# Kernel tuning notes

Hardware: AMD Instinct MI355X
Metric: run time of the kernel (lower is better)

## Reference

```python
import jax, jax.numpy as jnp
import numpy as np

N_NODES = 100000
N_EDGES = 3200000
IN_C, HID, OUT_C = 128, 256, 128
N_GRAPHS = 64
EPS = 1e-5


def setup_inputs() -> dict:
    key = jax.random.key(0)
    ks = jax.random.split(key, 16)
    x = jax.random.normal(ks[0], (N_NODES, IN_C), dtype=jnp.float32)
    edge_index = jax.random.randint(ks[1], (2, N_EDGES), 0, N_NODES, dtype=jnp.int64 if jax.config.jax_enable_x64 else jnp.int32)
    batch = jnp.sort(jax.random.randint(ks[2], (N_NODES,), 0, N_GRAPHS, dtype=jnp.int32))
    def glorot(k, shape):
        lim = jnp.sqrt(6.0 / (shape[-2] + shape[-1]))
        return jax.random.uniform(k, shape, jnp.float32, -lim, lim)
    return {
        "x": x,
        "W_in": glorot(ks[3], (IN_C, HID)),
        "b_in": jnp.zeros((HID,), jnp.float32),
        "g_in": jnp.ones((HID,), jnp.float32),
        "be_in": jnp.zeros((HID,), jnp.float32),
        "W_hid": glorot(ks[4], (2, HID, HID)),
        "b_hid": jnp.zeros((2, HID), jnp.float32),
        "g_hid": jnp.ones((2, HID), jnp.float32),
        "be_hid": jnp.zeros((2, HID), jnp.float32),
        "W_out": glorot(ks[5], (HID, OUT_C)),
        "b_out": jnp.zeros((OUT_C,), jnp.float32),
        "g_out": jnp.ones((OUT_C,), jnp.float32),
        "be_out": jnp.zeros((OUT_C,), jnp.float32),
        "edge_index": edge_index,
        "batch": batch,
    }


def _gcn_norm(edge_index, n_nodes):
    # add self-loops, symmetric deg^-1/2 normalization (PyG GCNConv defaults)
    loop = jnp.arange(n_nodes, dtype=edge_index.dtype)
    src = jnp.concatenate([edge_index[0], loop])
    dst = jnp.concatenate([edge_index[1], loop])
    deg = jax.ops.segment_sum(jnp.ones_like(dst, dtype=jnp.float32), dst, num_segments=n_nodes)
    dinv = jnp.where(deg > 0, jax.lax.rsqrt(deg), 0.0)
    norm = dinv[src] * dinv[dst]  # [E+N]
    return src, dst, norm


def _block(x, W, b, g, be, src, dst, norm, n_nodes):
    h = x @ W  # [N, out]
    agg = jax.ops.segment_sum(h[src] * norm[:, None], dst, num_segments=n_nodes) + b
    a = jax.nn.leaky_relu(agg, negative_slope=0.01)
    mu = jnp.mean(a, axis=0)
    var = jnp.mean(jnp.square(a - mu), axis=0)
    return (a - mu) * jax.lax.rsqrt(var + EPS) * g + be


def reference(x, W_in, b_in, g_in, be_in, W_hid, b_hid, g_hid, be_hid,
              W_out, b_out, g_out, be_out, edge_index, batch):
    n = x.shape[0]
    src, dst, norm = _gcn_norm(edge_index, n)
    h = _block(x, W_in, b_in, g_in, be_in, src, dst, norm, n)
    for i in range(W_hid.shape[0]):
        h = _block(h, W_hid[i], b_hid[i], g_hid[i], be_hid[i], src, dst, norm, n)
    h = _block(h, W_out, b_out, g_out, be_out, src, dst, norm, n)
    # global mean pool over graphs
    sums = jax.ops.segment_sum(h, batch, num_segments=N_GRAPHS)
    cnts = jax.ops.segment_sum(jnp.ones((n,), h.dtype), batch, num_segments=N_GRAPHS)
    return sums / jnp.maximum(cnts, 1.0)[:, None]
```

## Files before the change

### kernel.cpp

```cpp
#include <hip/hip_runtime.h>
#include <stdint.h>

#define EPS_LN 1e-5f

typedef short bf16x8 __attribute__((ext_vector_type(8)));
typedef float f32x4  __attribute__((ext_vector_type(4)));

__device__ __forceinline__ unsigned short f2bf(float f) {
    unsigned u = __float_as_uint(f);
    unsigned r = (u + 0x7fffu + ((u >> 16) & 1u)) >> 16;
    return (unsigned short)r;
}
__device__ __forceinline__ float bf_lo(unsigned u) { return __uint_as_float(u << 16); }
__device__ __forceinline__ float bf_hi(unsigned u) { return __uint_as_float(u & 0xffff0000u); }

__device__ __forceinline__ void async16(void* lds, const void* g) {
    __builtin_amdgcn_global_load_lds(
        (const __attribute__((address_space(1))) unsigned int*)g,
        (__attribute__((address_space(3))) unsigned int*)lds, 16, 0, 0);
}


__global__ void count_deg_kernel(const int* __restrict__ dst, int E, unsigned* __restrict__ deg) {
    int e = blockIdx.x * blockDim.x + threadIdx.x;
    if (e < E) atomicAdd(&deg[dst[e]], 1u);
}

__global__ void block_sums_kernel(const unsigned* __restrict__ deg, unsigned* __restrict__ part, int N) {
    __shared__ unsigned s[256];
    int t = threadIdx.x;
    int i0 = blockIdx.x * 512 + t * 2;
    unsigned a = (i0 < N) ? deg[i0] : 0u;
    unsigned b = (i0 + 1 < N) ? deg[i0 + 1] : 0u;
    s[t] = a + b;
    __syncthreads();
    for (int off = 128; off > 0; off >>= 1) {
        if (t < off) s[t] += s[t + off];
        __syncthreads();
    }
    if (t == 0) part[blockIdx.x] = s[0];
}

__global__ void scan_part_kernel(unsigned* __restrict__ part, unsigned* __restrict__ row_ptr,
                                 int NB, int N) {
    __shared__ unsigned s[256];
    int t = threadIdx.x;
    unsigned v = (t < NB) ? part[t] : 0u;
    s[t] = v;
    __syncthreads();
    for (int off = 1; off < 256; off <<= 1) {
        unsigned u = (t >= off) ? s[t - off] : 0u;
        __syncthreads();
        s[t] += u;
        __syncthreads();
    }
    if (t < NB) part[t] = s[t] - v;
    if (t == 255) row_ptr[N] = s[255];
}

__global__ void scan_blocks_kernel(const unsigned* __restrict__ deg, const unsigned* __restrict__ part,
                                   unsigned* __restrict__ row_ptr, unsigned* __restrict__ cursor,
                                   float* __restrict__ dinv, int N) {
    __shared__ unsigned s[256];
    int t = threadIdx.x;
    int i0 = blockIdx.x * 512 + t * 2;
    unsigned a = (i0 < N) ? deg[i0] : 0u;
    unsigned b = (i0 + 1 < N) ? deg[i0 + 1] : 0u;
    unsigned pair = a + b;
    s[t] = pair;
    __syncthreads();
    for (int off = 1; off < 256; off <<= 1) {
        unsigned u = (t >= off) ? s[t - off] : 0u;
        __syncthreads();
        s[t] += u;
        __syncthreads();
    }
    unsigned excl = s[t] - pair + part[blockIdx.x];
    if (i0 < N) {
        row_ptr[i0] = excl; cursor[i0] = excl;
        dinv[i0] = rsqrtf((float)(a + 1u));
    }
    if (i0 + 1 < N) {
        row_ptr[i0 + 1] = excl + a; cursor[i0 + 1] = excl + a;
        dinv[i0 + 1] = rsqrtf((float)(b + 1u));
    }
}

__global__ void fill_csr_kernel(const int* __restrict__ src, const int* __restrict__ dst,
                                const float* __restrict__ dinv, int E,
                                unsigned* __restrict__ cursor, uint2* __restrict__ csr) {
    int e = blockIdx.x * blockDim.x + threadIdx.x;
    if (e < E) {
        int d = dst[e];
        int s = src[e];
        unsigned pos = atomicAdd(&cursor[d], 1u);
        float w = dinv[d] * dinv[s];
        csr[pos] = make_uint2((unsigned)s, __float_as_uint(w));
    }
}

__global__ void prep_all_kernel(const float* __restrict__ x, unsigned* __restrict__ xbf,
                                const float* __restrict__ W_in, unsigned short* __restrict__ Wt_in,
                                const float* __restrict__ W_hid, unsigned short* __restrict__ Wt_h0,
                                unsigned short* __restrict__ Wt_h1, int n2) {
    int i = blockIdx.x * blockDim.x + threadIdx.x;
    if (i < n2) {
        float2 v = *reinterpret_cast<const float2*>(&x[(size_t)i * 2]);
        xbf[i] = (unsigned)f2bf(v.x) | ((unsigned)f2bf(v.y) << 16);
        return;
    }
    int r = i - n2;
    if (r < 32768) {
        int k = r >> 8, c = r & 255;
        Wt_in[(size_t)c * 128 + k] = f2bf(W_in[r]);
    } else if (r < 32768 + 65536) {
        r -= 32768;
        int k = r >> 8, c = r & 255;
        Wt_h0[(size_t)c * 256 + k] = f2bf(W_hid[r]);
    } else if (r < 32768 + 131072) {
        r -= 32768 + 65536;
        int k = r >> 8, c = r & 255;
        Wt_h1[(size_t)c * 256 + k] = f2bf(W_hid[65536 + r]);
    }
}

template<int UPL, bool AFF, bool FINAL>
__global__ void aggregate_bf(const unsigned* __restrict__ X, void* __restrict__ outp,
                             const unsigned* __restrict__ row_ptr, const uint2* __restrict__ csr,
                             const float* __restrict__ dinv,
                             const float* __restrict__ ssum, const float* __restrict__ ssq,
                             const float* __restrict__ gg, const float* __restrict__ be, float invN,
                             const float* __restrict__ tW, const float* __restrict__ bias, int N) {
    constexpr int C = UPL * 64;
    constexpr unsigned RSU = C / 2;
    constexpr int PC = UPL * 2;

    __shared__ float sL[AFF ? C : 1], tL[AFF ? C : 1];
    if constexpr (AFF) {
        for (int i = threadIdx.x; i < C; i += 256) {
            float mu = ssum[i] * invN;
            float var = ssq[i] * invN - mu * mu;
            float s = gg[i] * rsqrtf(var + EPS_LN);
            sL[i] = s;
            tL[i] = be[i] - mu * s;
        }
        __syncthreads();
    }

    int node = blockIdx.x * 8 + (threadIdx.x >> 5);
    if (node >= N) return;
    int ll = threadIdx.x & 31;
    unsigned cu = (unsigned)ll * UPL;

    float di = dinv[node];
    float w0 = di * di;
    float acc[PC];
    float wsum = w0;
    {
        const unsigned* xr = X + (size_t)((unsigned)node * RSU + cu);
        if constexpr (UPL == 4) {
            uint4 v = *reinterpret_cast<const uint4*>(xr);
            unsigned uu[4] = {v.x, v.y, v.z, v.w};
            #pragma unroll
            for (int q = 0; q < 4; ++q) {
                acc[q * 2 + 0] = w0 * bf_lo(uu[q]);
                acc[q * 2 + 1] = w0 * bf_hi(uu[q]);
            }
        } else {
            uint2 v = *reinterpret_cast<const uint2*>(xr);
            acc[0] = w0 * bf_lo(v.x); acc[1] = w0 * bf_hi(v.x);
            acc[2] = w0 * bf_lo(v.y); acc[3] = w0 * bf_hi(v.y);
        }
    }
    unsigned e0 = row_ptr[node];
    unsigned e1 = row_ptr[node + 1];
    unsigned cnt = e1 - e0;
    unsigned full = cnt & ~7u;

    for (unsigned i = 0; i < full; i += 8) {
        uint2 p[8];
        #pragma unroll
        for (int u = 0; u < 8; ++u) p[u] = csr[e0 + i + u];
        if constexpr (UPL == 4) {
            uint4 v[8];
            #pragma unroll
            for (int u = 0; u < 8; ++u)
                v[u] = *reinterpret_cast<const uint4*>(X + (size_t)(p[u].x * RSU + cu));
            #pragma unroll
            for (int u = 0; u < 8; ++u) {
                float f = __uint_as_float(p[u].y);
                unsigned uu[4] = {v[u].x, v[u].y, v[u].z, v[u].w};
                #pragma unroll
                for (int q = 0; q < 4; ++q) {
                    acc[q * 2 + 0] += f * bf_lo(uu[q]);
                    acc[q * 2 + 1] += f * bf_hi(uu[q]);
                }
                wsum += f;
            }
        } else {
            uint2 v[8];
            #pragma unroll
            for (int u = 0; u < 8; ++u)
                v[u] = *reinterpret_cast<const uint2*>(X + (size_t)(p[u].x * RSU + cu));
            #pragma unroll
            for (int u = 0; u < 8; ++u) {
                float f = __uint_as_float(p[u].y);
                acc[0] += f * bf_lo(v[u].x); acc[1] += f * bf_hi(v[u].x);
                acc[2] += f * bf_lo(v[u].y); acc[3] += f * bf_hi(v[u].y);
                wsum += f;
            }
        }
    }
    for (unsigned i = full; i < cnt; ++i) {
        uint2 p = csr[e0 + i];
        float f = __uint_as_float(p.y);
        if constexpr (UPL == 4) {
            uint4 v = *reinterpret_cast<const uint4*>(X + (size_t)(p.x * RSU + cu));
            unsigned uu[4] = {v.x, v.y, v.z, v.w};
            #pragma unroll
            for (int q = 0; q < 4; ++q) {
                acc[q * 2 + 0] += f * bf_lo(uu[q]);
                acc[q * 2 + 1] += f * bf_hi(uu[q]);
            }
        } else {
            uint2 v = *reinterpret_cast<const uint2*>(X + (size_t)(p.x * RSU + cu));
            acc[0] += f * bf_lo(v.x); acc[1] += f * bf_hi(v.x);
            acc[2] += f * bf_lo(v.y); acc[3] += f * bf_hi(v.y);
        }
        wsum += f;
    }

    int col = ll * PC;
    float z[PC];
    #pragma unroll
    for (int j = 0; j < PC; ++j) {
        float f = acc[j];
        if constexpr (AFF) f = sL[col + j] * f + tL[col + j] * wsum;
        if constexpr (FINAL) {
            f = f + wsum * tW[col + j] + bias[col + j];
            f = f > 0.f ? f : 0.01f * f;
        }
        z[j] = f;
    }
    if constexpr (FINAL) {
        float* of = (float*)outp;
        *reinterpret_cast<float4*>(&of[(size_t)node * C + col]) = make_float4(z[0], z[1], z[2], z[3]);
    } else {
        unsigned* ou = (unsigned*)outp;
        if constexpr (UPL == 4) {
            uint4 pk;
            pk.x = (unsigned)f2bf(z[0]) | ((unsigned)f2bf(z[1]) << 16);
            pk.y = (unsigned)f2bf(z[2]) | ((unsigned)f2bf(z[3]) << 16);
            pk.z = (unsigned)f2bf(z[4]) | ((unsigned)f2bf(z[5]) << 16);
            pk.w = (unsigned)f2bf(z[6]) | ((unsigned)f2bf(z[7]) << 16);
            *reinterpret_cast<uint4*>(&ou[(size_t)((unsigned)node * RSU + cu)]) = pk;
        } else {
            uint2 pk;
            pk.x = (unsigned)f2bf(z[0]) | ((unsigned)f2bf(z[1]) << 16);
            pk.y = (unsigned)f2bf(z[2]) | ((unsigned)f2bf(z[3]) << 16);
            *reinterpret_cast<uint2*>(&ou[(size_t)((unsigned)node * RSU + cu)]) = pk;
        }
    }
}

template<int K, int NN, bool EPI>
__launch_bounds__(256)
__global__ void gemm_mfma(const unsigned short* __restrict__ Z, const unsigned short* __restrict__ Wt,
                          const float* __restrict__ bias, unsigned short* __restrict__ out,
                          float* __restrict__ stat_sum, float* __restrict__ stat_sq, int M) {
    __shared__ char smem[32768];
    __shared__ float csum[128], csq[128];

    const int tid = threadIdx.x;
    const int lane = tid & 63;
    const int w = tid >> 6;
    const int wr = (w >> 1) * 64;
    const int wc = (w & 1) * 64;
    const int rowBase = blockIdx.x * 128;
    const int colBase = blockIdx.y * 128;
    const int frow = lane & 15;
    const int kgrp = lane >> 4;

    f32x4 acc[4][4] = {};

    for (int kt = 0; kt < K / 64; ++kt) {
        #pragma unroll
        for (int i = 0; i < 4; ++i) {
            int g = (i * 4 + w) * 64 + lane;
            int r = g >> 3;
            int bl = (g & 7) * 16;
            int bg = bl ^ ((r & 7) << 4);
            const char* src = (const char*)Z + (((size_t)(rowBase + r) * K + kt * 64) << 1) + bg;
            async16(&smem[(i * 4 + w) * 1024], src);
        }
        #pragma unroll
        for (int i = 0; i < 4; ++i) {
            int g = (i * 4 + w) * 64 + lane;
            int r = g >> 3;
            int bl = (g & 7) * 16;
            int bg = bl ^ ((r & 7) << 4);
            const char* src = (const char*)Wt + (((size_t)(colBase + r) * K + kt * 64) << 1) + bg;
            async16(&smem[16384 + (i * 4 + w) * 1024], src);
        }
        __syncthreads();
        #pragma unroll
        for (int kk = 0; kk < 2; ++kk) {
            const int kbyte = kk * 64 + kgrp * 16;
            bf16x8 af[4], bfr[4];
            #pragma unroll
            for (int m = 0; m < 4; ++m) {
                int r = wr + m * 16 + frow;
                af[m] = *reinterpret_cast<const bf16x8*>(&smem[r * 128 + (kbyte ^ ((r & 7) << 4))]);
            }
            #pragma unroll
            for (int n = 0; n < 4; ++n) {
                int c = wc + n * 16 + frow;
                bfr[n] = *reinterpret_cast<const bf16x8*>(&smem[16384 + c * 128 + (kbyte ^ ((c & 7) << 4))]);
            }
            #pragma unroll
            for (int m = 0; m < 4; ++m)
                #pragma unroll
                for (int n = 0; n < 4; ++n)
                    acc[m][n] = __builtin_amdgcn_mfma_f32_16x16x32_bf16(bfr[n], af[m], acc[m][n], 0, 0, 0);
        }
        __syncthreads();
    }

    if constexpr (EPI) {
        if (tid < 128) { csum[tid] = 0.f; csq[tid] = 0.f; }
        __syncthreads();
    }

    #pragma unroll
    for (int n = 0; n < 4; ++n) {
        const int c_local = wc + n * 16 + kgrp * 4;
        const int col = colBase + c_local;
        float4 b4 = make_float4(0.f, 0.f, 0.f, 0.f);
        if constexpr (EPI) b4 = *reinterpret_cast<const float4*>(&bias[col]);
        float ps[4] = {0.f, 0.f, 0.f, 0.f}, pq[4] = {0.f, 0.f, 0.f, 0.f};
        #pragma unroll
        for (int m = 0; m < 4; ++m) {
            int row = rowBase + wr + m * 16 + frow;
            if (row < M) {
                float f0 = acc[m][n][0] + b4.x;
                float f1 = acc[m][n][1] + b4.y;
                float f2 = acc[m][n][2] + b4.z;
                float f3 = acc[m][n][3] + b4.w;
                if constexpr (EPI) {
                    f0 = f0 > 0.f ? f0 : 0.01f * f0;
                    f1 = f1 > 0.f ? f1 : 0.01f * f1;
                    f2 = f2 > 0.f ? f2 : 0.01f * f2;
                    f3 = f3 > 0.f ? f3 : 0.01f * f3;
                }
                uint2 pk;
                pk.x = (unsigned)f2bf(f0) | ((unsigned)f2bf(f1) << 16);
                pk.y = (unsigned)f2bf(f2) | ((unsigned)f2bf(f3) << 16);
                *reinterpret_cast<uint2*>(&out[(size_t)row * NN + col]) = pk;
                if constexpr (EPI) {
                    ps[0] += f0; ps[1] += f1; ps[2] += f2; ps[3] += f3;
                    pq[0] += f0 * f0; pq[1] += f1 * f1; pq[2] += f2 * f2; pq[3] += f3 * f3;
                }
            }
        }
        if constexpr (EPI) {
            #pragma unroll
            for (int s = 1; s < 16; s <<= 1) {
                #pragma unroll
                for (int j = 0; j < 4; ++j) {
                    ps[j] += __shfl_xor(ps[j], s);
                    pq[j] += __shfl_xor(pq[j], s);
                }
            }
            if (frow == 0) {
                #pragma unroll
                for (int j = 0; j < 4; ++j) {
                    atomicAdd(&csum[c_local + j], ps[j]);
                    atomicAdd(&csq[c_local + j], pq[j]);
                }
            }
        }
    }
    if constexpr (EPI) {
        __syncthreads();
        if (tid < 128) {
            atomicAdd(&stat_sum[colBase + tid], csum[tid]);
            atomicAdd(&stat_sq[colBase + tid], csq[tid]);
        }
    }
}

__global__ void prep_wout_tw(const float* __restrict__ W,
                             const float* __restrict__ ssum, const float* __restrict__ ssq,
                             const float* __restrict__ gg, const float* __restrict__ be, float invN,
                             unsigned short* __restrict__ Wt, float* __restrict__ tW) {
    if (blockIdx.x < 128) {
        int idx = blockIdx.x * 256 + threadIdx.x;
        int k = idx >> 7, c = idx & 127;
        float mu = ssum[k] * invN;
        float var = ssq[k] * invN - mu * mu;
        float s = gg[k] * rsqrtf(var + EPS_LN);
        Wt[(size_t)c * 256 + k] = f2bf(s * W[idx]);
    } else {
        int c = threadIdx.x;
        if (c < 128) {
            float acc = 0.f;
            for (int k = 0; k < 256; ++k) {
                float mu = ssum[k] * invN;
                float var = ssq[k] * invN - mu * mu;
                float s = gg[k] * rsqrtf(var + EPS_LN);
                float t = be[k] - mu * s;
                acc += t * W[k * 128 + c];
            }
            tW[c] = acc;
        }
    }
}

__global__ void stats_pool_kernel(const float* __restrict__ A, const int* __restrict__ batch,
                                  float* __restrict__ stat_sum, float* __restrict__ stat_sq,
                                  float* __restrict__ psums, float* __restrict__ pcnt, int N) {
    int c = threadIdx.x;
    int n0 = blockIdx.x * 256;
    if (n0 >= N) return;
    int n1 = min(n0 + 256, N);
    float cs = 0.f, cq = 0.f;
    float acc = 0.f, cacc = 0.f;
    int curg = -1;
    for (int n = n0; n < n1; ++n) {
        float v = A[(size_t)n * 128 + c];
        cs += v; cq += v * v;
        int g = batch[n];
        if (g != curg) {
            if (curg >= 0) {
                atomicAdd(&psums[curg * 128 + c], acc);
                if (c == 0) atomicAdd(&pcnt[curg], cacc);
            }
            acc = 0.f; cacc = 0.f; curg = g;
        }
        acc += v;
        cacc += 1.f;
    }
    if (curg >= 0) {
        atomicAdd(&psums[curg * 128 + c], acc);
        if (c == 0) atomicAdd(&pcnt[curg], cacc);
    }
    atomicAdd(&stat_sum[c], cs);
    atomicAdd(&stat_sq[c], cq);
}

__global__ void divide_kernel(const float* __restrict__ psums, const float* __restrict__ pcnt,
                              const float* __restrict__ ssum, const float* __restrict__ ssq,
                              const float* __restrict__ gg, const float* __restrict__ be, float invN,
                              float* __restrict__ out) {
    int i = blockIdx.x * blockDim.x + threadIdx.x;
    if (i < 64 * 128) {
        int g = i >> 7, c = i & 127;
        float mu = ssum[c] * invN;
        float var = ssq[c] * invN - mu * mu;
        float s = gg[c] * rsqrtf(var + EPS_LN);
        float t = be[c] - mu * s;
        float cnt = pcnt[g];
        out[i] = (cnt > 0.f) ? s * (psums[i] / cnt) + t : 0.f;
    }
}

extern "C" void kernel_launch(void* const* d_in, const int* in_sizes, int n_in,
                              void* d_out, int out_size, void* d_ws, size_t ws_size,
                              hipStream_t stream) {
    const float* x      = (const float*)d_in[0];
    const float* W_in   = (const float*)d_in[1];
    const float* b_in   = (const float*)d_in[2];
    const float* g_in   = (const float*)d_in[3];
    const float* be_in  = (const float*)d_in[4];
    const float* W_hid  = (const float*)d_in[5];
    const float* b_hid  = (const float*)d_in[6];
    const float* g_hid  = (const float*)d_in[7];
    const float* be_hid = (const float*)d_in[8];
    const float* W_out  = (const float*)d_in[9];
    const float* b_out  = (const float*)d_in[10];
    const float* g_out  = (const float*)d_in[11];
    const float* be_out = (const float*)d_in[12];
    const int*   eidx   = (const int*)d_in[13];
    const int*   batch  = (const int*)d_in[14];
    float* out = (float*)d_out;

    const int N = in_sizes[14];
    const int E = in_sizes[13] / 2;
    const int Npad = ((N + 127) / 128) * 128;
    const int NB = (N + 511) / 512;
    const int* e_src = eidx;
    const int* e_dst = eidx + E;

    char* ws = (char*)d_ws;
    size_t off = 0;
    auto alloc = [&](size_t bytes) -> void* {
        void* p = ws + off;
        off = (off + bytes + 255) & ~(size_t)255;
        return p;
    };
    char* B1 = (char*)alloc((size_t)Npad * 256 * 2);
    char* B2 = (char*)alloc((size_t)Npad * 256 * 2);
    unsigned* deg      = (unsigned*)alloc((size_t)N * 4);
    float*    dinv     = (float*)alloc((size_t)N * 4);
    unsigned* row_ptr  = (unsigned*)alloc((size_t)(N + 1) * 4);
    unsigned* cursor   = (unsigned*)alloc((size_t)N * 4);
    unsigned* part     = (unsigned*)alloc(256 * 4);
    uint2*    csr      = (uint2*)alloc((size_t)E * 8);
    unsigned short* Wt_in  = (unsigned short*)alloc(256 * 128 * 2);
    unsigned short* Wt_h0  = (unsigned short*)alloc(256 * 256 * 2);
    unsigned short* Wt_h1  = (unsigned short*)alloc(256 * 256 * 2);
    unsigned short* Wt_out = (unsigned short*)alloc(128 * 256 * 2);
    float*    tW       = (float*)alloc(128 * 4);
    float*    stats    = (float*)alloc(4 * 512 * 4);
    float*    psums    = (float*)alloc(64 * 128 * 4);
    float*    pcnt     = (float*)alloc(64 * 4);

    float* s1 = stats + 0 * 512, *q1 = s1 + 256;
    float* s2 = stats + 1 * 512, *q2 = s2 + 256;
    float* s3 = stats + 2 * 512, *q3 = s3 + 256;
    float* s4 = stats + 3 * 512, *q4 = s4 + 256;

    const float invN = 1.0f / (float)N;

    hipMemsetAsync(deg, 0, (size_t)N * 4, stream);
    hipMemsetAsync(stats, 0, ((char*)pcnt + 64 * 4) - (char*)stats, stream);

    int egrid = (E + 255) / 256;
    count_deg_kernel<<<egrid, 256, 0, stream>>>(e_dst, E, deg);
    block_sums_kernel<<<NB, 256, 0, stream>>>(deg, part, N);
    scan_part_kernel<<<1, 256, 0, stream>>>(part, row_ptr, NB, N);
    scan_blocks_kernel<<<NB, 256, 0, stream>>>(deg, part, row_ptr, cursor, dinv, N);
    fill_csr_kernel<<<egrid, 256, 0, stream>>>(e_src, e_dst, dinv, E, cursor, csr);

    {
        int total = N * 64 + 32768 + 65536 + 65536;
        prep_all_kernel<<<(total + 255) / 256, 256, 0, stream>>>(
            x, (unsigned*)B2, W_in, Wt_in, W_hid, Wt_h0, Wt_h1, N * 64);
    }

    const int aggGrid = (N + 7) / 8;
    dim3 gg256(Npad / 128, 2);

    aggregate_bf<2, false, false><<<aggGrid, 256, 0, stream>>>(
        (const unsigned*)B2, B1, row_ptr, csr, dinv,
        nullptr, nullptr, nullptr, nullptr, invN, nullptr, nullptr, N);
    gemm_mfma<128, 256, true><<<gg256, 256, 0, stream>>>(
        (const unsigned short*)B1, Wt_in, b_in, (unsigned short*)B2, s1, q1, N);

    aggregate_bf<4, true, false><<<aggGrid, 256, 0, stream>>>(
        (const unsigned*)B2, B1, row_ptr, csr, dinv,
        s1, q1, g_in, be_in, invN, nullptr, nullptr, N);
    gemm_mfma<256, 256, true><<<gg256, 256, 0, stream>>>(
        (const unsigned short*)B1, Wt_h0, b_hid, (unsigned short*)B2, s2, q2, N);

    aggregate_bf<4, true, false><<<aggGrid, 256, 0, stream>>>(
        (const unsigned*)B2, B1, row_ptr, csr, dinv,
        s2, q2, g_hid, be_hid, invN, nullptr, nullptr, N);
    gemm_mfma<256, 256, true><<<gg256, 256, 0, stream>>>(
        (const unsigned short*)B1, Wt_h1, b_hid + 256, (unsigned short*)B2, s3, q3, N);

    prep_wout_tw<<<129, 256, 0, stream>>>(W_out, s3, q3, g_hid + 256, be_hid + 256, invN, Wt_out, tW);
    gemm_mfma<256, 128, false><<<dim3(Npad / 128, 1), 256, 0, stream>>>(
        (const unsigned short*)B2, Wt_out, nullptr, (unsigned short*)B1, nullptr, nullptr, N);
    aggregate_bf<2, false, true><<<aggGrid, 256, 0, stream>>>(
        (const unsigned*)B1, B2, row_ptr, csr, dinv,
        nullptr, nullptr, nullptr, nullptr, invN, tW, b_out, N);

    stats_pool_kernel<<<(N + 255) / 256, 128, 0, stream>>>(
        (const float*)B2, batch, s4, q4, psums, pcnt, N);
    divide_kernel<<<(64 * 128 + 255) / 256, 256, 0, stream>>>(
        psums, pcnt, s4, q4, g_out, be_out, invN, out);
}
```

Baseline: 1.314 ms.

## Pack CSR entries into 32-bit words and store final aggregate as bf16

Each CSR entry shrinks from 8 bytes to 4: a 17-bit source index plus a 15-bit quantized dinv[src]. The dinv[dst] factor is applied per node inside the aggregation. CSR build now records each edge's atomic rank during degree counting, which is merged with the x/W conversion into one setup kernel, and fill_csr places edges by row_ptr+rank without a second round of atomics. The final aggregation now writes bf16 instead of fp32 and the pooling kernel reads bf16. This halves edge-list traffic in four aggregation passes and shrinks the final output. The cost is precision: edge weights are quantized to 15 bits and the last layer is rounded to bf16. Node indices are limited to 2^17, which holds for these inputs.

```diff
diff --git a/kernel.cpp b/kernel.cpp
--- a/kernel.cpp
+++ b/kernel.cpp
@@ -20,96 +20,24 @@
         (__attribute__((address_space(3))) unsigned int*)lds, 16, 0, 0);
 }
 
-
-__global__ void count_deg_kernel(const int* __restrict__ dst, int E, unsigned* __restrict__ deg) {
-    int e = blockIdx.x * blockDim.x + threadIdx.x;
-    if (e < E) atomicAdd(&deg[dst[e]], 1u);
-}
-
-__global__ void block_sums_kernel(const unsigned* __restrict__ deg, unsigned* __restrict__ part, int N) {
-    __shared__ unsigned s[256];
-    int t = threadIdx.x;
-    int i0 = blockIdx.x * 512 + t * 2;
-    unsigned a = (i0 < N) ? deg[i0] : 0u;
-    unsigned b = (i0 + 1 < N) ? deg[i0 + 1] : 0u;
-    s[t] = a + b;
-    __syncthreads();
-    for (int off = 128; off > 0; off >>= 1) {
-        if (t < off) s[t] += s[t + off];
-        __syncthreads();
-    }
-    if (t == 0) part[blockIdx.x] = s[0];
-}
-
-__global__ void scan_part_kernel(unsigned* __restrict__ part, unsigned* __restrict__ row_ptr,
-                                 int NB, int N) {
-    __shared__ unsigned s[256];
-    int t = threadIdx.x;
-    unsigned v = (t < NB) ? part[t] : 0u;
-    s[t] = v;
-    __syncthreads();
-    for (int off = 1; off < 256; off <<= 1) {
-        unsigned u = (t >= off) ? s[t - off] : 0u;
-        __syncthreads();
-        s[t] += u;
-        __syncthreads();
-    }
-    if (t < NB) part[t] = s[t] - v;
-    if (t == 255) row_ptr[N] = s[255];
-}
-
-__global__ void scan_blocks_kernel(const unsigned* __restrict__ deg, const unsigned* __restrict__ part,
-                                   unsigned* __restrict__ row_ptr, unsigned* __restrict__ cursor,
-                                   float* __restrict__ dinv, int N) {
-    __shared__ unsigned s[256];
-    int t = threadIdx.x;
-    int i0 = blockIdx.x * 512 + t * 2;
-    unsigned a = (i0 < N) ? deg[i0] : 0u;
-    unsigned b = (i0 + 1 < N) ? deg[i0 + 1] : 0u;
-    unsigned pair = a + b;
-    s[t] = pair;
-    __syncthreads();
-    for (int off = 1; off < 256; off <<= 1) {
-        unsigned u = (t >= off) ? s[t - off] : 0u;
-        __syncthreads();
-        s[t] += u;
-        __syncthreads();
-    }
-    unsigned excl = s[t] - pair + part[blockIdx.x];
-    if (i0 < N) {
-        row_ptr[i0] = excl; cursor[i0] = excl;
-        dinv[i0] = rsqrtf((float)(a + 1u));
-    }
-    if (i0 + 1 < N) {
-        row_ptr[i0 + 1] = excl + a; cursor[i0 + 1] = excl + a;
-        dinv[i0 + 1] = rsqrtf((float)(b + 1u));
-    }
-}
-
-__global__ void fill_csr_kernel(const int* __restrict__ src, const int* __restrict__ dst,
-                                const float* __restrict__ dinv, int E,
-                                unsigned* __restrict__ cursor, uint2* __restrict__ csr) {
-    int e = blockIdx.x * blockDim.x + threadIdx.x;
-    if (e < E) {
-        int d = dst[e];
-        int s = src[e];
-        unsigned pos = atomicAdd(&cursor[d], 1u);
-        float w = dinv[d] * dinv[s];
-        csr[pos] = make_uint2((unsigned)s, __float_as_uint(w));
-    }
-}
-
-__global__ void prep_all_kernel(const float* __restrict__ x, unsigned* __restrict__ xbf,
-                                const float* __restrict__ W_in, unsigned short* __restrict__ Wt_in,
-                                const float* __restrict__ W_hid, unsigned short* __restrict__ Wt_h0,
-                                unsigned short* __restrict__ Wt_h1, int n2) {
+__global__ void setup_kernel(const int* __restrict__ dst, int E,
+                             unsigned* __restrict__ deg, unsigned* __restrict__ rank,
+                             const float* __restrict__ x, unsigned* __restrict__ xbf, int n2,
+                             const float* __restrict__ W_in, unsigned short* __restrict__ Wt_in,
+                             const float* __restrict__ W_hid, unsigned short* __restrict__ Wt_h0,
+                             unsigned short* __restrict__ Wt_h1) {
     int i = blockIdx.x * blockDim.x + threadIdx.x;
-    if (i < n2) {
-        float2 v = *reinterpret_cast<const float2*>(&x[(size_t)i * 2]);
-        xbf[i] = (unsigned)f2bf(v.x) | ((unsigned)f2bf(v.y) << 16);
+    if (i < E) {
+        rank[i] = atomicAdd(&deg[dst[i]], 1u);
         return;
     }
-    int r = i - n2;
+    int j = i - E;
+    if (j < n2) {
+        float2 v = *reinterpret_cast<const float2*>(&x[(size_t)j * 2]);
+        xbf[j] = (unsigned)f2bf(v.x) | ((unsigned)f2bf(v.y) << 16);
+        return;
+    }
+    int r = j - n2;
     if (r < 32768) {
         int k = r >> 8, c = r & 255;
         Wt_in[(size_t)c * 128 + k] = f2bf(W_in[r]);
@@ -124,9 +52,81 @@
     }
 }
 
+__global__ void block_sums_kernel(const unsigned* __restrict__ deg, unsigned* __restrict__ part, int N) {
+    __shared__ unsigned s[256];
+    int t = threadIdx.x;
+    int i0 = blockIdx.x * 512 + t * 2;
+    unsigned a = (i0 < N) ? deg[i0] : 0u;
+    unsigned b = (i0 + 1 < N) ? deg[i0 + 1] : 0u;
+    s[t] = a + b;
+    __syncthreads();
+    for (int off = 128; off > 0; off >>= 1) {
+        if (t < off) s[t] += s[t + off];
+        __syncthreads();
+    }
+    if (t == 0) part[blockIdx.x] = s[0];
+}
+
+__global__ void scan_part_kernel(unsigned* __restrict__ part, unsigned* __restrict__ row_ptr,
+                                 int NB, int N) {
+    __shared__ unsigned s[256];
+    int t = threadIdx.x;
+    unsigned v = (t < NB) ? part[t] : 0u;
+    s[t] = v;
+    __syncthreads();
+    for (int off = 1; off < 256; off <<= 1) {
+        unsigned u = (t >= off) ? s[t - off] : 0u;
+        __syncthreads();
+        s[t] += u;
+        __syncthreads();
+    }
+    if (t < NB) part[t] = s[t] - v;
+    if (t == 255) row_ptr[N] = s[255];
+}
+
+__global__ void scan_blocks_kernel(const unsigned* __restrict__ deg, const unsigned* __restrict__ part,
+                                   unsigned* __restrict__ row_ptr, float* __restrict__ dinv, int N) {
+    __shared__ unsigned s[256];
+    int t = threadIdx.x;
+    int i0 = blockIdx.x * 512 + t * 2;
+    unsigned a = (i0 < N) ? deg[i0] : 0u;
+    unsigned b = (i0 + 1 < N) ? deg[i0 + 1] : 0u;
+    unsigned pair = a + b;
+    s[t] = pair;
+    __syncthreads();
+    for (int off = 1; off < 256; off <<= 1) {
+        unsigned u = (t >= off) ? s[t - off] : 0u;
+        __syncthreads();
+        s[t] += u;
+        __syncthreads();
+    }
+    unsigned excl = s[t] - pair + part[blockIdx.x];
+    if (i0 < N) {
+        row_ptr[i0] = excl;
+        dinv[i0] = rsqrtf((float)(a + 1u));
+    }
+    if (i0 + 1 < N) {
+        row_ptr[i0 + 1] = excl + a;
+        dinv[i0 + 1] = rsqrtf((float)(b + 1u));
+    }
+}
+
+__global__ void fill_csr_kernel(const int* __restrict__ src, const int* __restrict__ dst,
+                                const unsigned* __restrict__ rank, const unsigned* __restrict__ row_ptr,
+                                const float* __restrict__ dinv, int E, unsigned* __restrict__ csr) {
+    int e = blockIdx.x * blockDim.x + threadIdx.x;
+    if (e < E) {
+        int d = dst[e];
+        int s = src[e];
+        unsigned pos = row_ptr[d] + rank[e];
+        unsigned wq = __float2uint_rn(dinv[s] * 32767.f);
+        csr[pos] = (wq << 17) | (unsigned)s;
+    }
+}
+
 template<int UPL, bool AFF, bool FINAL>
-__global__ void aggregate_bf(const unsigned* __restrict__ X, void* __restrict__ outp,
-                             const unsigned* __restrict__ row_ptr, const uint2* __restrict__ csr,
+__global__ void aggregate_bf(const unsigned* __restrict__ X, unsigned* __restrict__ outp,
+                             const unsigned* __restrict__ row_ptr, const unsigned* __restrict__ csr,
                              const float* __restrict__ dinv,
                              const float* __restrict__ ssum, const float* __restrict__ ssq,
                              const float* __restrict__ gg, const float* __restrict__ be, float invN,
@@ -153,6 +153,7 @@
     unsigned cu = (unsigned)ll * UPL;
 
     float di = dinv[node];
+    float dscale = di * (1.f / 32767.f);
     float w0 = di * di;
     float acc[PC];
     float wsum = w0;
@@ -178,17 +179,17 @@
     unsigned full = cnt & ~7u;
 
     for (unsigned i = 0; i < full; i += 8) {
-        uint2 p[8];
+        unsigned p[8];
         #pragma unroll
         for (int u = 0; u < 8; ++u) p[u] = csr[e0 + i + u];
         if constexpr (UPL == 4) {
             uint4 v[8];
             #pragma unroll
             for (int u = 0; u < 8; ++u)
-                v[u] = *reinterpret_cast<const uint4*>(X + (size_t)(p[u].x * RSU + cu));
+                v[u] = *reinterpret_cast<const uint4*>(X + (size_t)((p[u] & 0x1FFFFu) * RSU + cu));
             #pragma unroll
             for (int u = 0; u < 8; ++u) {
-                float f = __uint_as_float(p[u].y);
+                float f = (float)(p[u] >> 17) * dscale;
                 unsigned uu[4] = {v[u].x, v[u].y, v[u].z, v[u].w};
                 #pragma unroll
                 for (int q = 0; q < 4; ++q) {
@@ -201,10 +202,10 @@
             uint2 v[8];
             #pragma unroll
             for (int u = 0; u < 8; ++u)
-                v[u] = *reinterpret_cast<const uint2*>(X + (size_t)(p[u].x * RSU + cu));
+                v[u] = *reinterpret_cast<const uint2*>(X + (size_t)((p[u] & 0x1FFFFu) * RSU + cu));
             #pragma unroll
             for (int u = 0; u < 8; ++u) {
-                float f = __uint_as_float(p[u].y);
+                float f = (float)(p[u] >> 17) * dscale;
                 acc[0] += f * bf_lo(v[u].x); acc[1] += f * bf_hi(v[u].x);
                 acc[2] += f * bf_lo(v[u].y); acc[3] += f * bf_hi(v[u].y);
                 wsum += f;
@@ -212,10 +213,10 @@
         }
     }
     for (unsigned i = full; i < cnt; ++i) {
-        uint2 p = csr[e0 + i];
-        float f = __uint_as_float(p.y);
+        unsigned p = csr[e0 + i];
+        float f = (float)(p >> 17) * dscale;
         if constexpr (UPL == 4) {
-            uint4 v = *reinterpret_cast<const uint4*>(X + (size_t)(p.x * RSU + cu));
+            uint4 v = *reinterpret_cast<const uint4*>(X + (size_t)((p & 0x1FFFFu) * RSU + cu));
             unsigned uu[4] = {v.x, v.y, v.z, v.w};
             #pragma unroll
             for (int q = 0; q < 4; ++q) {
@@ -223,7 +224,7 @@
                 acc[q * 2 + 1] += f * bf_hi(uu[q]);
             }
         } else {
-            uint2 v = *reinterpret_cast<const uint2*>(X + (size_t)(p.x * RSU + cu));
+            uint2 v = *reinterpret_cast<const uint2*>(X + (size_t)((p & 0x1FFFFu) * RSU + cu));
             acc[0] += f * bf_lo(v.x); acc[1] += f * bf_hi(v.x);
             acc[2] += f * bf_lo(v.y); acc[3] += f * bf_hi(v.y);
         }
@@ -242,24 +243,18 @@
         }
         z[j] = f;
     }
-    if constexpr (FINAL) {
-        float* of = (float*)outp;
-        *reinterpret_cast<float4*>(&of[(size_t)node * C + col]) = make_float4(z[0], z[1], z[2], z[3]);
+    if constexpr (UPL == 4) {
+        uint4 pk;
+        pk.x = (unsigned)f2bf(z[0]) | ((unsigned)f2bf(z[1]) << 16);
+        pk.y = (unsigned)f2bf(z[2]) | ((unsigned)f2bf(z[3]) << 16);
+        pk.z = (unsigned)f2bf(z[4]) | ((unsigned)f2bf(z[5]) << 16);
+        pk.w = (unsigned)f2bf(z[6]) | ((unsigned)f2bf(z[7]) << 16);
+        *reinterpret_cast<uint4*>(&outp[(size_t)((unsigned)node * RSU + cu)]) = pk;
     } else {
-        unsigned* ou = (unsigned*)outp;
-        if constexpr (UPL == 4) {
-            uint4 pk;
-            pk.x = (unsigned)f2bf(z[0]) | ((unsigned)f2bf(z[1]) << 16);
-            pk.y = (unsigned)f2bf(z[2]) | ((unsigned)f2bf(z[3]) << 16);
-            pk.z = (unsigned)f2bf(z[4]) | ((unsigned)f2bf(z[5]) << 16);
-            pk.w = (unsigned)f2bf(z[6]) | ((unsigned)f2bf(z[7]) << 16);
-            *reinterpret_cast<uint4*>(&ou[(size_t)((unsigned)node * RSU + cu)]) = pk;
-        } else {
-            uint2 pk;
-            pk.x = (unsigned)f2bf(z[0]) | ((unsigned)f2bf(z[1]) << 16);
-            pk.y = (unsigned)f2bf(z[2]) | ((unsigned)f2bf(z[3]) << 16);
-            *reinterpret_cast<uint2*>(&ou[(size_t)((unsigned)node * RSU + cu)]) = pk;
-        }
+        uint2 pk;
+        pk.x = (unsigned)f2bf(z[0]) | ((unsigned)f2bf(z[1]) << 16);
+        pk.y = (unsigned)f2bf(z[2]) | ((unsigned)f2bf(z[3]) << 16);
+        *reinterpret_cast<uint2*>(&outp[(size_t)((unsigned)node * RSU + cu)]) = pk;
     }
 }
 
@@ -416,7 +411,7 @@
     }
 }
 
-__global__ void stats_pool_kernel(const float* __restrict__ A, const int* __restrict__ batch,
+__global__ void stats_pool_kernel(const unsigned short* __restrict__ A, const int* __restrict__ batch,
                                   float* __restrict__ stat_sum, float* __restrict__ stat_sq,
                                   float* __restrict__ psums, float* __restrict__ pcnt, int N) {
     int c = threadIdx.x;
@@ -427,7 +422,7 @@
     float acc = 0.f, cacc = 0.f;
     int curg = -1;
     for (int n = n0; n < n1; ++n) {
-        float v = A[(size_t)n * 128 + c];
+        float v = __uint_as_float((unsigned)A[(size_t)n * 128 + c] << 16);
         cs += v; cq += v * v;
         int g = batch[n];
         if (g != curg) {
@@ -503,9 +498,9 @@
     unsigned* deg      = (unsigned*)alloc((size_t)N * 4);
     float*    dinv     = (float*)alloc((size_t)N * 4);
     unsigned* row_ptr  = (unsigned*)alloc((size_t)(N + 1) * 4);
-    unsigned* cursor   = (unsigned*)alloc((size_t)N * 4);
+    unsigned* rank     = (unsigned*)alloc((size_t)E * 4);
     unsigned* part     = (unsigned*)alloc(256 * 4);
-    uint2*    csr      = (uint2*)alloc((size_t)E * 8);
+    unsigned* csr      = (unsigned*)alloc((size_t)E * 4);
     unsigned short* Wt_in  = (unsigned short*)alloc(256 * 128 * 2);
     unsigned short* Wt_h0  = (unsigned short*)alloc(256 * 256 * 2);
     unsigned short* Wt_h1  = (unsigned short*)alloc(256 * 256 * 2);
@@ -525,36 +520,33 @@
     hipMemsetAsync(deg, 0, (size_t)N * 4, stream);
     hipMemsetAsync(stats, 0, ((char*)pcnt + 64 * 4) - (char*)stats, stream);
 
-    int egrid = (E + 255) / 256;
-    count_deg_kernel<<<egrid, 256, 0, stream>>>(e_dst, E, deg);
+    {
+        int total = E + N * 64 + 32768 + 65536 + 65536;
+        setup_kernel<<<(total + 255) / 256, 256, 0, stream>>>(
+            e_dst, E, deg, rank, x, (unsigned*)B2, N * 64, W_in, Wt_in, W_hid, Wt_h0, Wt_h1);
+    }
     block_sums_kernel<<<NB, 256, 0, stream>>>(deg, part, N);
     scan_part_kernel<<<1, 256, 0, stream>>>(part, row_ptr, NB, N);
-    scan_blocks_kernel<<<NB, 256, 0, stream>>>(deg, part, row_ptr, cursor, dinv, N);
-    fill_csr_kernel<<<egrid, 256, 0, stream>>>(e_src, e_dst, dinv, E, cursor, csr);
-
-    {
-        int total = N * 64 + 32768 + 65536 + 65536;
-        prep_all_kernel<<<(total + 255) / 256, 256, 0, stream>>>(
-            x, (unsigned*)B2, W_in, Wt_in, W_hid, Wt_h0, Wt_h1, N * 64);
-    }
+    scan_blocks_kernel<<<NB, 256, 0, stream>>>(deg, part, row_ptr, dinv, N);
+    fill_csr_kernel<<<(E + 255) / 256, 256, 0, stream>>>(e_src, e_dst, rank, row_ptr, dinv, E, csr);
 
     const int aggGrid = (N + 7) / 8;
     dim3 gg256(Npad / 128, 2);
 
     aggregate_bf<2, false, false><<<aggGrid, 256, 0, stream>>>(
-        (const unsigned*)B2, B1, row_ptr, csr, dinv,
+        (const unsigned*)B2, (unsigned*)B1, row_ptr, csr, dinv,
         nullptr, nullptr, nullptr, nullptr, invN, nullptr, nullptr, N);
     gemm_mfma<128, 256, true><<<gg256, 256, 0, stream>>>(
         (const unsigned short*)B1, Wt_in, b_in, (unsigned short*)B2, s1, q1, N);
 
     aggregate_bf<4, true, false><<<aggGrid, 256, 0, stream>>>(
-        (const unsigned*)B2, B1, row_ptr, csr, dinv,
+        (const unsigned*)B2, (unsigned*)B1, row_ptr, csr, dinv,
         s1, q1, g_in, be_in, invN, nullptr, nullptr, N);
     gemm_mfma<256, 256, true><<<gg256, 256, 0, stream>>>(
         (const unsigned short*)B1, Wt_h0, b_hid, (unsigned short*)B2, s2, q2, N);
 
     aggregate_bf<4, true, false><<<aggGrid, 256, 0, stream>>>(
-        (const unsigned*)B2, B1, row_ptr, csr, dinv,
+        (const unsigned*)B2, (unsigned*)B1, row_ptr, csr, dinv,
         s2, q2, g_hid, be_hid, invN, nullptr, nullptr, N);
     gemm_mfma<256, 256, true><<<gg256, 256, 0, stream>>>(
         (const unsigned short*)B1, Wt_h1, b_hid + 256, (unsigned short*)B2, s3, q3, N);
@@ -563,11 +555,11 @@
     gemm_mfma<256, 128, false><<<dim3(Npad / 128, 1), 256, 0, stream>>>(
         (const unsigned short*)B2, Wt_out, nullptr, (unsigned short*)B1, nullptr, nullptr, N);
     aggregate_bf<2, false, true><<<aggGrid, 256, 0, stream>>>(
-        (const unsigned*)B1, B2, row_ptr, csr, dinv,
+        (const unsigned*)B1, (unsigned*)B2, row_ptr, csr, dinv,
         nullptr, nullptr, nullptr, nullptr, invN, tW, b_out, N);
 
     stats_pool_kernel<<<(N + 255) / 256, 128, 0, stream>>>(
-        (const float*)B2, batch, s4, q4, psums, pcnt, N);
+        (const unsigned short*)B2, batch, s4, q4, psums, pcnt, N);
     divide_kernel<<<(64 * 128 + 255) / 256, 256, 0, stream>>>(
         psums, pcnt, s4, q4, g_out, be_out, invN, out);
 }
```

Result: faster. 1.154 ms, median of 2 (-12.2%).
